# Performance work log

Hardware: AMD Instinct MI355X
Metric: run time of the kernel (lower is better)

## Reference

```python
import jax, jax.numpy as jnp
import numpy as np

N = 100000
E = 1000000
D = 32          # numerical_dim
HID = 64        # hidden_dim
OUT = 1         # output_dim
REL = 4 * D     # relation feature dim
EPS = 1e-8


def setup_inputs() -> dict:
    key = jax.random.key(0)
    k_x, k_e, k_w1, k_b1, k_w2, k_b2 = jax.random.split(key, 6)
    x = jax.random.uniform(k_x, (N, D), dtype=jnp.float32)
    edge_index = jax.random.randint(k_e, (2, E), 0, N, dtype=jnp.int64)
    # Linear params (PyTorch convention: W [out, in], y = x @ W.T + b)
    lim1 = 1.0 / np.sqrt(REL)
    W1 = jax.random.uniform(k_w1, (HID, REL), minval=-lim1, maxval=lim1, dtype=jnp.float32)
    b1 = jax.random.uniform(k_b1, (HID,), minval=-lim1, maxval=lim1, dtype=jnp.float32)
    lim2 = 1.0 / np.sqrt(HID)
    W2 = jax.random.uniform(k_w2, (OUT, HID), minval=-lim2, maxval=lim2, dtype=jnp.float32)
    b2 = jax.random.uniform(k_b2, (OUT,), minval=-lim2, maxval=lim2, dtype=jnp.float32)
    return {"x": x, "edge_index": edge_index, "W1": W1, "b1": b1, "W2": W2, "b2": b2}


def _relation_features(x_i, x_j):
    ratio = x_i / (x_j + EPS)
    log_ratio = jnp.log(x_i + EPS) - jnp.log(x_j + EPS)
    abs_diff = jnp.abs(x_i - x_j)
    rel_diff = abs_diff / (jnp.maximum(x_i, x_j) + EPS)
    return jnp.concatenate([ratio, log_ratio, abs_diff, rel_diff], axis=-1)  # [E, 4D]


def reference(x, edge_index, W1, b1, W2, b2):
    src, dst = edge_index[0], edge_index[1]
    x_i = x[src]                      # [E, D] gather source node feats
    x_j = x[dst]                      # [E, D] gather target node feats
    rel = _relation_features(x_i, x_j)  # [E, 4D]
    h = jax.nn.relu(rel @ W1.T + b1)    # [E, HID]
    edge_bias = (h @ W2.T + b2).squeeze(-1)  # [E]
    return edge_bias
```

## Files before the change

kernel.cpp:

```cpp
#include <hip/hip_runtime.h>


#define DD    32
#define HID   64
#define RELF  128
#define EPSF  1e-8f
#define LXLO  -18.420681f
#define LXSC  13.843137f
#define LXIV  0.07223796f
#define MSC   3.0517578125e-05f

typedef short  bf16x8 __attribute__((ext_vector_type(8)));
typedef float  f32x4  __attribute__((ext_vector_type(4)));

union U8 { unsigned u[4]; bf16x8 v; uint4 q4; };
union Q  { uint4 v; unsigned u[4]; float f[4]; };

static __device__ __forceinline__ unsigned pk_tr(float lo, float hi) {
    return __builtin_amdgcn_perm(__builtin_bit_cast(unsigned, hi),
                                 __builtin_bit_cast(unsigned, lo), 0x07060302u);
}
static __device__ __forceinline__ unsigned rne_bits(float f) {
    unsigned u = __builtin_bit_cast(unsigned, f);
    return u + 0x7fffu + ((u >> 16) & 1u);
}
static __device__ __forceinline__ unsigned pk_rne(float lo, float hi) {
    return __builtin_amdgcn_perm(rne_bits(hi), rne_bits(lo), 0x07060302u);
}
static __device__ __forceinline__ float hi_f32(float f) {
    return __builtin_bit_cast(float, __builtin_bit_cast(unsigned, f) & 0xffff0000u);
}
static __device__ __forceinline__ float ubyte(unsigned w, int b) {
    return (float)((w >> (8 * b)) & 0xffu);
}
static __device__ __forceinline__ unsigned q8(float v) {
    int u = (int)(v + 0.5f);
    return (unsigned)(u > 255 ? 255 : (u < 0 ? 0 : u));
}
template <int CTRL>
static __device__ __forceinline__ float dpp_ror_add(float pp) {
    int s = __builtin_bit_cast(int, pp);
    int t = __builtin_amdgcn_update_dpp(0, s, CTRL, 0xf, 0xf, true);
    return pp + __builtin_bit_cast(float, t);
}

__global__ __launch_bounds__(256)
void prep_pack(const float* __restrict__ x, uint4* __restrict__ rec, int nchunk)
{
    int i = blockIdx.x * blockDim.x + threadIdx.x;
    if (i >= nchunk) return;
    const float4* xp = (const float4*)(x + (size_t)i * 8);
    float4 v0 = xp[0], v1 = xp[1];
    float xv[8] = {v0.x, v0.y, v0.z, v0.w, v1.x, v1.y, v1.z, v1.w};

    unsigned xh[4];
    #pragma unroll
    for (int p = 0; p < 4; ++p) xh[p] = pk_tr(xv[2*p], xv[2*p+1]);

    unsigned xl[2] = {0u, 0u}, lu[2] = {0u, 0u};
    #pragma unroll
    for (int e = 0; e < 8; ++e) {
        float a  = xv[e];
        float ah = hi_f32(a);
        float f  = 0.f;
        if (ah > 0.f)
            f = (a * __builtin_amdgcn_rcpf(ah) - 1.f) * 32768.f;
        xl[e >> 2] |= q8(f) << (8 * (e & 3));
        float lxe = __logf(a + EPSF);
        lu[e >> 2] |= q8((lxe - LXLO) * LXSC) << (8 * (e & 3));
    }

    uint4 r0; r0.x = xh[0]; r0.y = xh[1]; r0.z = xh[2]; r0.w = xh[3];
    uint4 r1; r1.x = xl[0]; r1.y = xl[1]; r1.z = lu[0]; r1.w = lu[1];
    rec[2 * i]     = r0;
    rec[2 * i + 1] = r1;
}

template <int PACK>
__global__ __launch_bounds__(256, 4)
void edge_bias_mfma(const float* __restrict__ x,
                    const int*   __restrict__ ei,
                    const float* __restrict__ W1,
                    const float* __restrict__ b1,
                    const float* __restrict__ W2,
                    const float* __restrict__ b2,
                    const uint4* __restrict__ rec,
                    float* __restrict__ out,
                    int E)
{
    const int lane = threadIdx.x & 63;
    const int wv   = threadIdx.x >> 6;
    const int wave = (blockIdx.x * blockDim.x + threadIdx.x) >> 6;
    const int nwv  = (gridDim.x * blockDim.x) >> 6;
    const int c = lane & 15;
    const int q = lane >> 4;

    __shared__ uint4 sW[20 * 64];
    for (int s = wv; s < 5; s += 4) {
        #pragma unroll
        for (int nt = 0; nt < 4; ++nt) {
            const float* wr = W1 + (nt * 16 + c) * RELF + q * 8;
            U8 t;
            if (s == 0) {
                #pragma unroll
                for (int p = 0; p < 4; ++p)
                    t.u[p] = pk_tr(wr[2*p], wr[2*p+1]);
            } else if (s == 1) {
                #pragma unroll
                for (int p = 0; p < 4; ++p) {
                    float w0 = wr[2*p], w1 = wr[2*p+1];
                    t.u[p] = pk_rne(w0 - hi_f32(w0), w1 - hi_f32(w1));
                }
            } else {
                const int base = (s == 2) ? 32 : (s == 3) ? 64 : 96;
                #pragma unroll
                for (int p = 0; p < 4; ++p)
                    t.u[p] = pk_rne(wr[base + 2*p], wr[base + 2*p + 1]);
            }
            sW[(s * 4 + nt) * 64 + lane] = t.q4;
        }
    }
    __syncthreads();

    float b1v[4], w2v[4];
    #pragma unroll
    for (int nt = 0; nt < 4; ++nt) {
        b1v[nt] = b1[nt * 16 + c];
        w2v[nt] = W2[nt * 16 + c];
    }
    const float b2s = b2[0];

    const int ntiles = (E + 15) >> 4;
    int t = wave;
    if (t >= ntiles) return;

    auto ldidx = [&](int tt_, int& s, int& d) {
        if (tt_ >= ntiles) tt_ = t;
        int em = (tt_ << 4) + c; if (em > E - 1) em = E - 1;
        s = ei[em]; d = ei[E + em];
    };
    auto gather = [&](int s, int d, Q& hi_, Q& mi_, Q& hj_, Q& mj_) {
        if constexpr (PACK) {
            const uint4* pi = rec + (size_t)s * 8 + q * 2;
            const uint4* pj = rec + (size_t)d * 8 + q * 2;
            hi_.v = pi[0]; mi_.v = pi[1];
            hj_.v = pj[0]; mj_.v = pj[1];
        } else {
            const uint4* pi = (const uint4*)(x + (size_t)s * DD + q * 8);
            const uint4* pj = (const uint4*)(x + (size_t)d * DD + q * 8);
            hi_.v = pi[0]; mi_.v = pi[1];
            hj_.v = pj[0]; mj_.v = pj[1];
        }
    };
    auto decode = [&](const Q& h, const Q& m, float* xv, bf16x8& lfrag) {
        #pragma unroll
        for (int p = 0; p < 4; ++p) {
            float lo = __builtin_bit_cast(float, h.u[p] << 16);
            float hi = __builtin_bit_cast(float, h.u[p] & 0xffff0000u);
            unsigned xb = (p < 2) ? m.u[0] : m.u[1];
            float m0 = ubyte(xb, (2 * p) & 3);
            float m1 = ubyte(xb, (2 * p + 1) & 3);
            xv[2 * p]     = fmaf(lo * MSC, m0, lo);
            xv[2 * p + 1] = fmaf(hi * MSC, m1, hi);
        }
        U8 L;
        #pragma unroll
        for (int p = 0; p < 4; ++p) {
            unsigned lb = (p < 2) ? m.u[2] : m.u[3];
            float l0 = fmaf(ubyte(lb, (2 * p) & 3),     LXIV, LXLO);
            float l1 = fmaf(ubyte(lb, (2 * p + 1) & 3), LXIV, LXLO);
            L.u[p] = pk_tr(l0, l1);
        }
        lfrag = L.v;
    };

    auto compute = [&](int tc, const Q& hI, const Q& mI, const Q& hJ, const Q& mJ) {
        float xiv[8], xjv[8];
        bf16x8 aLi, aLj;
        if constexpr (PACK) {
            decode(hI, mI, xiv, aLi);
            decode(hJ, mJ, xjv, aLj);
        } else {
            #pragma unroll
            for (int p = 0; p < 4; ++p) { xiv[p] = hI.f[p]; xiv[4 + p] = mI.f[p]; }
            #pragma unroll
            for (int p = 0; p < 4; ++p) { xjv[p] = hJ.f[p]; xjv[4 + p] = mJ.f[p]; }
            U8 ti, tj;
            #pragma unroll
            for (int p = 0; p < 4; ++p) {
                ti.u[p] = pk_rne(__logf(xiv[2*p] + EPSF), __logf(xiv[2*p+1] + EPSF));
                tj.u[p] = pk_rne(__logf(xjv[2*p] + EPSF), __logf(xjv[2*p+1] + EPSF));
            }
            aLi = ti.v; aLj = tj.v;
        }
        U8 nj; nj.v = aLj;
        #pragma unroll
        for (int p = 0; p < 4; ++p) nj.u[p] ^= 0x80008000u;

        U8 R, Rl, Aa, Dd;
        #pragma unroll
        for (int p = 0; p < 4; ++p) {
            float a0 = xiv[2*p], a1 = xiv[2*p+1];
            float c0 = xjv[2*p], c1 = xjv[2*p+1];
            float r0 = a0 * __builtin_amdgcn_rcpf(c0 + EPSF);
            float r1 = a1 * __builtin_amdgcn_rcpf(c1 + EPSF);
            float d0 = fabsf(a0 - c0), d1 = fabsf(a1 - c1);
            float g0 = d0 * __builtin_amdgcn_rcpf(fmaxf(a0, c0) + EPSF);
            float g1 = d1 * __builtin_amdgcn_rcpf(fmaxf(a1, c1) + EPSF);
            R.u[p]  = pk_tr(r0, r1);
            Rl.u[p] = pk_tr(r0 - hi_f32(r0), r1 - hi_f32(r1));
            Aa.u[p] = pk_tr(d0, d1);
            Dd.u[p] = pk_tr(g0, g1);
        }

        int off = lane;
        asm volatile("" : "+v"(off));
        auto ldfrag = [&](int s, int nt) {
            U8 w; w.q4 = sW[(s * 4 + nt) * 64 + off];
            return w.v;
        };

        f32x4 acc[4];
        #pragma unroll
        for (int nt = 0; nt < 4; ++nt) {
            acc[nt][0] = b1v[nt]; acc[nt][1] = b1v[nt];
            acc[nt][2] = b1v[nt]; acc[nt][3] = b1v[nt];
        }
        #pragma unroll
        for (int nt = 0; nt < 4; ++nt) {
            bf16x8 fW0h = ldfrag(0, nt);
            bf16x8 fW0l = ldfrag(1, nt);
            bf16x8 fWL  = ldfrag(2, nt);
            bf16x8 fWA  = ldfrag(3, nt);
            bf16x8 fWD  = ldfrag(4, nt);
            acc[nt] = __builtin_amdgcn_mfma_f32_16x16x32_bf16(R.v,  fW0h, acc[nt], 0, 0, 0);
            acc[nt] = __builtin_amdgcn_mfma_f32_16x16x32_bf16(Rl.v, fW0h, acc[nt], 0, 0, 0);
            acc[nt] = __builtin_amdgcn_mfma_f32_16x16x32_bf16(R.v,  fW0l, acc[nt], 0, 0, 0);
            acc[nt] = __builtin_amdgcn_mfma_f32_16x16x32_bf16(aLi,  fWL,  acc[nt], 0, 0, 0);
            acc[nt] = __builtin_amdgcn_mfma_f32_16x16x32_bf16(nj.v, fWL,  acc[nt], 0, 0, 0);
            acc[nt] = __builtin_amdgcn_mfma_f32_16x16x32_bf16(Aa.v, fWA,  acc[nt], 0, 0, 0);
            acc[nt] = __builtin_amdgcn_mfma_f32_16x16x32_bf16(Dd.v, fWD,  acc[nt], 0, 0, 0);
        }

        float p4[4];
        #pragma unroll
        for (int r = 0; r < 4; ++r) {
            float pp = 0.f;
            #pragma unroll
            for (int nt = 0; nt < 4; ++nt)
                pp = fmaf(fmaxf(acc[nt][r], 0.f), w2v[nt], pp);
            pp = dpp_ror_add<0x121>(pp);
            pp = dpp_ror_add<0x122>(pp);
            pp = dpp_ror_add<0x124>(pp);
            pp = dpp_ror_add<0x128>(pp);
            p4[r] = pp;
        }
        if (c < 4) {
            const int e = (tc << 4) + q * 4 + c;
            if (e < E) {
                float v = (c == 0) ? p4[0] : (c == 1) ? p4[1] : (c == 2) ? p4[2] : p4[3];
                out[e] = v + b2s;
            }
        }
    };

    Q hA, mA, hJA, mJA;
    Q hB, mB, hJB, mJB;
    int sC, dC;

    { int s, d; ldidx(t,        s, d); gather(s, d, hA, mA, hJA, mJA); }
    { int s, d; ldidx(t + nwv,  s, d); gather(s, d, hB, mB, hJB, mJB); }
    ldidx(t + 2 * nwv, sC, dC);

    for (;;) {
        compute(t, hA, mA, hJA, mJA);
        gather(sC, dC, hA, mA, hJA, mJA);
        ldidx(t + 3 * nwv, sC, dC);
        t += nwv; if (t >= ntiles) break;

        compute(t, hB, mB, hJB, mJB);
        gather(sC, dC, hB, mB, hJB, mJB);
        ldidx(t + 3 * nwv, sC, dC);
        t += nwv; if (t >= ntiles) break;
    }
}

extern "C" void kernel_launch(void* const* d_in, const int* in_sizes, int n_in,
                              void* d_out, int out_size, void* d_ws, size_t ws_size,
                              hipStream_t stream)
{
    const float* x   = (const float*)d_in[0];
    const int*   ei  = (const int*)  d_in[1];
    const float* W1  = (const float*)d_in[2];
    const float* b1  = (const float*)d_in[3];
    const float* W2  = (const float*)d_in[4];
    const float* b2  = (const float*)d_in[5];
    float* out = (float*)d_out;

    const int E  = out_size;
    const int Nd = in_sizes[0];
    uint4* rec = (uint4*)d_ws;

    const bool pack = ws_size >= (size_t)Nd * 4 && (Nd % 8) == 0;
    if (pack) {
        const int nchunk = Nd / 8;
        prep_pack<<<(nchunk + 255) / 256, 256, 0, stream>>>(x, rec, nchunk);
        edge_bias_mfma<1><<<2048, 256, 0, stream>>>(x, ei, W1, b1, W2, b2, rec, out, E);
    } else {
        edge_bias_mfma<0><<<2048, 256, 0, stream>>>(x, ei, W1, b1, W2, b2, rec, out, E);
    }
}
```

Before: 131.6 us.

## Keep W1 fragments in registers and drop software-pipelined gather prefetch

Loads all 20 W1 bf16 fragments from LDS into registers once per wave instead of reloading them from shared memory on every tile. To make room for the extra VGPRs, it removes the two-deep register prefetch of index and gather loads, falls back to a simple grid-stride loop, and lowers launch bounds from 4 to 3 waves per SIMD. This saves LDS reads per tile but gives up latency hiding for the random gathers and some occupancy, so the kernel may become more exposed to memory latency.

Result: slower. 165.9 us (+26.0%).

```diff
diff --git a/kernel.cpp b/kernel.cpp
--- a/kernel.cpp
+++ b/kernel.cpp
@@ -77,7 +77,7 @@
 }
 
 template <int PACK>
-__global__ __launch_bounds__(256, 4)
+__global__ __launch_bounds__(256, 3)
 void edge_bias_mfma(const float* __restrict__ x,
                     const int*   __restrict__ ei,
                     const float* __restrict__ W1,
@@ -122,6 +122,17 @@
     }
     __syncthreads();
 
+    bf16x8 wW0h[4], wW0l[4], wWL[4], wWA[4], wWD[4];
+    #pragma unroll
+    for (int nt = 0; nt < 4; ++nt) {
+        U8 w;
+        w.q4 = sW[(0 * 4 + nt) * 64 + lane]; wW0h[nt] = w.v;
+        w.q4 = sW[(1 * 4 + nt) * 64 + lane]; wW0l[nt] = w.v;
+        w.q4 = sW[(2 * 4 + nt) * 64 + lane]; wWL[nt]  = w.v;
+        w.q4 = sW[(3 * 4 + nt) * 64 + lane]; wWA[nt]  = w.v;
+        w.q4 = sW[(4 * 4 + nt) * 64 + lane]; wWD[nt]  = w.v;
+    }
+
     float b1v[4], w2v[4];
     #pragma unroll
     for (int nt = 0; nt < 4; ++nt) {
@@ -130,28 +141,6 @@
     }
     const float b2s = b2[0];
 
-    const int ntiles = (E + 15) >> 4;
-    int t = wave;
-    if (t >= ntiles) return;
-
-    auto ldidx = [&](int tt_, int& s, int& d) {
-        if (tt_ >= ntiles) tt_ = t;
-        int em = (tt_ << 4) + c; if (em > E - 1) em = E - 1;
-        s = ei[em]; d = ei[E + em];
-    };
-    auto gather = [&](int s, int d, Q& hi_, Q& mi_, Q& hj_, Q& mj_) {
-        if constexpr (PACK) {
-            const uint4* pi = rec + (size_t)s * 8 + q * 2;
-            const uint4* pj = rec + (size_t)d * 8 + q * 2;
-            hi_.v = pi[0]; mi_.v = pi[1];
-            hj_.v = pj[0]; mj_.v = pj[1];
-        } else {
-            const uint4* pi = (const uint4*)(x + (size_t)s * DD + q * 8);
-            const uint4* pj = (const uint4*)(x + (size_t)d * DD + q * 8);
-            hi_.v = pi[0]; mi_.v = pi[1];
-            hj_.v = pj[0]; mj_.v = pj[1];
-        }
-    };
     auto decode = [&](const Q& h, const Q& m, float* xv, bf16x8& lfrag) {
         #pragma unroll
         for (int p = 0; p < 4; ++p) {
@@ -174,7 +163,24 @@
         lfrag = L.v;
     };
 
-    auto compute = [&](int tc, const Q& hI, const Q& mI, const Q& hJ, const Q& mJ) {
+    const int ntiles = (E + 15) >> 4;
+    for (int t = wave; t < ntiles; t += nwv) {
+        int em = (t << 4) + c; if (em > E - 1) em = E - 1;
+        const int sn = ei[em], dn = ei[E + em];
+
+        Q hI, mI, hJ, mJ;
+        if constexpr (PACK) {
+            const uint4* pi = rec + (size_t)sn * 8 + q * 2;
+            const uint4* pj = rec + (size_t)dn * 8 + q * 2;
+            hI.v = pi[0]; mI.v = pi[1];
+            hJ.v = pj[0]; mJ.v = pj[1];
+        } else {
+            const uint4* pi = (const uint4*)(x + (size_t)sn * DD + q * 8);
+            const uint4* pj = (const uint4*)(x + (size_t)dn * DD + q * 8);
+            hI.v = pi[0]; mI.v = pi[1];
+            hJ.v = pj[0]; mJ.v = pj[1];
+        }
+
         float xiv[8], xjv[8];
         bf16x8 aLi, aLj;
         if constexpr (PACK) {
@@ -213,13 +219,6 @@
             Dd.u[p] = pk_tr(g0, g1);
         }
 
-        int off = lane;
-        asm volatile("" : "+v"(off));
-        auto ldfrag = [&](int s, int nt) {
-            U8 w; w.q4 = sW[(s * 4 + nt) * 64 + off];
-            return w.v;
-        };
-
         f32x4 acc[4];
         #pragma unroll
         for (int nt = 0; nt < 4; ++nt) {
@@ -228,18 +227,13 @@
         }
         #pragma unroll
         for (int nt = 0; nt < 4; ++nt) {
-            bf16x8 fW0h = ldfrag(0, nt);
-            bf16x8 fW0l = ldfrag(1, nt);
-            bf16x8 fWL  = ldfrag(2, nt);
-            bf16x8 fWA  = ldfrag(3, nt);
-            bf16x8 fWD  = ldfrag(4, nt);
-            acc[nt] = __builtin_amdgcn_mfma_f32_16x16x32_bf16(R.v,  fW0h, acc[nt], 0, 0, 0);
-            acc[nt] = __builtin_amdgcn_mfma_f32_16x16x32_bf16(Rl.v, fW0h, acc[nt], 0, 0, 0);
-            acc[nt] = __builtin_amdgcn_mfma_f32_16x16x32_bf16(R.v,  fW0l, acc[nt], 0, 0, 0);
-            acc[nt] = __builtin_amdgcn_mfma_f32_16x16x32_bf16(aLi,  fWL,  acc[nt], 0, 0, 0);
-            acc[nt] = __builtin_amdgcn_mfma_f32_16x16x32_bf16(nj.v, fWL,  acc[nt], 0, 0, 0);
-            acc[nt] = __builtin_amdgcn_mfma_f32_16x16x32_bf16(Aa.v, fWA,  acc[nt], 0, 0, 0);
-            acc[nt] = __builtin_amdgcn_mfma_f32_16x16x32_bf16(Dd.v, fWD,  acc[nt], 0, 0, 0);
+            acc[nt] = __builtin_amdgcn_mfma_f32_16x16x32_bf16(R.v,  wW0h[nt], acc[nt], 0, 0, 0);
+            acc[nt] = __builtin_amdgcn_mfma_f32_16x16x32_bf16(Rl.v, wW0h[nt], acc[nt], 0, 0, 0);
+            acc[nt] = __builtin_amdgcn_mfma_f32_16x16x32_bf16(R.v,  wW0l[nt], acc[nt], 0, 0, 0);
+            acc[nt] = __builtin_amdgcn_mfma_f32_16x16x32_bf16(aLi,  wWL[nt],  acc[nt], 0, 0, 0);
+            acc[nt] = __builtin_amdgcn_mfma_f32_16x16x32_bf16(nj.v, wWL[nt],  acc[nt], 0, 0, 0);
+            acc[nt] = __builtin_amdgcn_mfma_f32_16x16x32_bf16(Aa.v, wWA[nt],  acc[nt], 0, 0, 0);
+            acc[nt] = __builtin_amdgcn_mfma_f32_16x16x32_bf16(Dd.v, wWD[nt],  acc[nt], 0, 0, 0);
         }
 
         float p4[4];
@@ -256,32 +250,12 @@
             p4[r] = pp;
         }
         if (c < 4) {
-            const int e = (tc << 4) + q * 4 + c;
+            const int e = (t << 4) + q * 4 + c;
             if (e < E) {
                 float v = (c == 0) ? p4[0] : (c == 1) ? p4[1] : (c == 2) ? p4[2] : p4[3];
                 out[e] = v + b2s;
             }
         }
-    };
-
-    Q hA, mA, hJA, mJA;
-    Q hB, mB, hJB, mJB;
-    int sC, dC;
-
-    { int s, d; ldidx(t,        s, d); gather(s, d, hA, mA, hJA, mJA); }
-    { int s, d; ldidx(t + nwv,  s, d); gather(s, d, hB, mB, hJB, mJB); }
-    ldidx(t + 2 * nwv, sC, dC);
-
-    for (;;) {
-        compute(t, hA, mA, hJA, mJA);
-        gather(sC, dC, hA, mA, hJA, mJA);
-        ldidx(t + 3 * nwv, sC, dC);
-        t += nwv; if (t >= ntiles) break;
-
-        compute(t, hB, mB, hJB, mJB);
-        gather(sC, dC, hB, mB, hJB, mJB);
-        ldidx(t + 3 * nwv, sC, dC);
-        t += nwv; if (t >= ntiles) break;
     }
 }
 
```
